# Performance work log

Measured on AMD Instinct MI355X. Metric: run time of the kernel, lower is better.

## Reference

```python
import jax, jax.numpy as jnp
import numpy as np

B, N, K, H = 8, 3072, 20, 64
NT = B * N            # 24576 total nodes
E = NT * 20           # 491520 GAT edges
HEADS = 4
BN_EPS = 1e-5


def setup_inputs() -> dict:
    key = jax.random.key(0)
    ks = jax.random.split(key, 16)
    rn = lambda k, shp, s=0.05: jax.random.normal(k, shp, dtype=jnp.float32) * s
    z = lambda shp: jnp.zeros(shp, dtype=jnp.float32)
    inp = {}
    inp["x"] = jax.random.normal(ks[0], (NT, 8), dtype=jnp.float32)
    inp["batch"] = jnp.repeat(jnp.arange(B, dtype=jnp.int32), N)
    inp["edge_index"] = jax.random.randint(ks[1], (2, E), 0, NT)
    # lc_encode: Linear(8,32) -> ELU -> Linear(32,H) -> ELU
    inp["enc_W1"] = rn(ks[2], (8, 32)); inp["enc_b1"] = z(32)
    inp["enc_W2"] = rn(ks[3], (32, H)); inp["enc_b2"] = z(H)
    # 3 DynamicEdgeConv MLPs: Linear(2H,H) -> ELU -> BatchNorm(eval) -> Dropout(eval=id)
    inp["conv_W"] = rn(ks[4], (3, 2 * H, H)); inp["conv_b"] = z((3, H))
    inp["bn_g"] = jnp.ones((3, H), jnp.float32); inp["bn_b"] = z((3, H))
    inp["bn_m"] = z((3, H)); inp["bn_v"] = jnp.ones((3, H), jnp.float32)
    # 2 GATConv layers: heads=4, concat=False (mean over heads)
    inp["gat_W"] = rn(ks[5], (2, H, HEADS * H))
    inp["gat_asrc"] = rn(ks[6], (2, HEADS, H))
    inp["gat_adst"] = rn(ks[7], (2, HEADS, H))
    inp["gat_bias"] = z((2, H))
    # output MLP: Linear(H,64) ELU Linear(64,32) ELU Linear(32,8)
    inp["out_W1"] = rn(ks[8], (H, 64)); inp["out_b1"] = z(64)
    inp["out_W2"] = rn(ks[9], (64, 32)); inp["out_b2"] = z(32)
    inp["out_W3"] = rn(ks[10], (32, 8)); inp["out_b3"] = z(8)
    return inp


def _knn_idx(x):
    # x: [B,N,H]; k nearest neighbors per graph, excluding self
    sq = jnp.sum(x * x, axis=-1)
    d = sq[:, :, None] + sq[:, None, :] - 2.0 * jnp.einsum('bnh,bmh->bnm', x, x)
    d = d + jnp.eye(N, dtype=x.dtype)[None] * 1e9
    _, idx = jax.lax.top_k(-d, K)
    return idx  # [B,N,K]


def _dyn_edge_conv(x, W, b, g, be, m, v):
    # x: [B,N,H]; EdgeConv message nn([x_i, x_j - x_i]), max-aggr over k neighbors
    idx = _knn_idx(x)
    xj = jax.vmap(lambda xb, ib: xb[ib])(x, idx)          # [B,N,K,H]
    xi = x[:, :, None, :]
    e = jnp.concatenate([jnp.broadcast_to(xi, xj.shape), xj - xi], axis=-1)  # [B,N,K,2H]
    h = jax.nn.elu(jnp.einsum('bnkf,fh->bnkh', e, W) + b)
    h = g * (h - m) * jax.lax.rsqrt(v + BN_EPS) + be      # BatchNorm1d (eval)
    return jnp.max(h, axis=2)                             # [B,N,H]


def _gat(x, ei, W, asrc, adst, bias):
    # x: [NT,H]; PyG GATConv, heads=4, concat=False, with self-loops
    xh = (x @ W).reshape(NT, HEADS, H)
    loops = jnp.arange(NT)
    src = jnp.concatenate([ei[0], loops])
    dst = jnp.concatenate([ei[1], loops])
    al_s = jnp.einsum('nhc,hc->nh', xh, asrc)
    al_d = jnp.einsum('nhc,hc->nh', xh, adst)
    alpha = jax.nn.leaky_relu(al_s[src] + al_d[dst], 0.2)  # [E+NT, HEADS]
    mx = jax.ops.segment_max(alpha, dst, num_segments=NT)
    ea = jnp.exp(alpha - mx[dst])
    den = jax.ops.segment_sum(ea, dst, num_segments=NT)
    a = ea / (den[dst] + 1e-16)
    out = jax.ops.segment_sum(xh[src] * a[:, :, None], dst, num_segments=NT)
    return out.mean(axis=1) + bias                        # concat=False -> head mean


def reference(x, batch, edge_index, enc_W1, enc_b1, enc_W2, enc_b2,
              conv_W, conv_b, bn_g, bn_b, bn_m, bn_v,
              gat_W, gat_asrc, gat_adst, gat_bias,
              out_W1, out_b1, out_W2, out_b2, out_W3, out_b3):
    # lc_encode (dropout layers are identity in eval mode)
    h = jax.nn.elu(jax.nn.elu(x @ enc_W1 + enc_b1) @ enc_W2 + enc_b2)
    hb = h.reshape(B, N, H)  # regular batch: node i belongs to graph i // N
    for i in range(3):
        hb = _dyn_edge_conv(hb, conv_W[i], conv_b[i], bn_g[i], bn_b[i], bn_m[i], bn_v[i]) + hb
    feats = hb.reshape(NT, H)
    x1 = _gat(feats, edge_index, gat_W[0], gat_asrc[0], gat_adst[0], gat_bias[0]) + feats
    x2 = _gat(x1, edge_index, gat_W[1], gat_asrc[1], gat_adst[1], gat_bias[1]) + x1
    o = jax.nn.elu(x2 @ out_W1 + out_b1)
    o = jax.nn.elu(o @ out_W2 + out_b2)
    return o @ out_W3 + out_b3  # [NT, contrastive_dim]
```

## Files before the change

### kernel.cpp

```cpp
#include <hip/hip_runtime.h>
#include <math.h>

#define NTOT  24576
#define NB    8
#define NPB   3072
#define HD    64
#define KNN   20
#define NTILE 24

__device__ __forceinline__ float elu_f(float x){ return x > 0.f ? x : expm1f(x); }

__global__ __launch_bounds__(256) void enc_kernel(const float* __restrict__ x,
    const float* __restrict__ W1, const float* __restrict__ b1,
    const float* __restrict__ W2, const float* __restrict__ b2,
    float* __restrict__ out, float* __restrict__ sqo){
  __shared__ float sW1[256], sb1[32], sW2[2048], sb2[64];
  int t = threadIdx.x;
  if (t < 256) sW1[t] = W1[t];
  for (int i = t; i < 2048; i += 256) sW2[i] = W2[i];
  if (t < 32) sb1[t] = b1[t];
  if (t < 64) sb2[t] = b2[t];
  __syncthreads();
  int n = blockIdx.x*256 + t;
  const float4* xp = (const float4*)(x + (size_t)n*8);
  float4 x0 = xp[0], x1 = xp[1];
  float xi[8] = {x0.x,x0.y,x0.z,x0.w,x1.x,x1.y,x1.z,x1.w};
  float h1[32];
  #pragma unroll
  for (int j = 0; j < 32; j++){
    float a = sb1[j];
    #pragma unroll
    for (int d = 0; d < 8; d++) a = fmaf(xi[d], sW1[d*32+j], a);
    h1[j] = elu_f(a);
  }
  float4* op = (float4*)(out + (size_t)n*64);
  float ssum = 0.f;
  #pragma unroll
  for (int c4 = 0; c4 < 16; c4++){
    float a0 = sb2[c4*4+0], a1 = sb2[c4*4+1], a2 = sb2[c4*4+2], a3 = sb2[c4*4+3];
    #pragma unroll
    for (int d = 0; d < 32; d++){
      float hd = h1[d];
      float4 wv = *(const float4*)&sW2[d*64 + c4*4];
      a0 = fmaf(hd, wv.x, a0); a1 = fmaf(hd, wv.y, a1);
      a2 = fmaf(hd, wv.z, a2); a3 = fmaf(hd, wv.w, a3);
    }
    float4 o; o.x=elu_f(a0); o.y=elu_f(a1); o.z=elu_f(a2); o.w=elu_f(a3);
    ssum = fmaf(o.x,o.x,ssum); ssum = fmaf(o.y,o.y,ssum);
    ssum = fmaf(o.z,o.z,ssum); ssum = fmaf(o.w,o.w,ssum);
    op[c4] = o;
  }
  sqo[n] = ssum;
}

#define CE(va,ia,vb,ib) { bool sw_ = (vb) < (va); float t1_ = sw_?(vb):(va); float t2_ = sw_?(va):(vb); int t3_ = sw_?(ib):(ia); int t4_ = sw_?(ia):(ib); (va)=t1_; (vb)=t2_; (ia)=t3_; (ib)=t4_; }

__global__ __launch_bounds__(256) void disttop_kernel(const float* __restrict__ feat,
    const float* __restrict__ sqn, float* __restrict__ topv, unsigned int* __restrict__ topi){
  __shared__ float As[16][128];
  __shared__ float Bs[16][128];
  int b  = blockIdx.z;
  int m0 = blockIdx.x * 128;
  int q0 = blockIdx.y * 128;
  const float* fb = feat + (size_t)b*NPB*HD;
  int t = threadIdx.x;
  int tx = t & 15, ty = t >> 4;
  float acc[8][8];
  #pragma unroll
  for (int i = 0; i < 8; i++)
    #pragma unroll
    for (int j = 0; j < 8; j++) acc[i][j] = 0.f;
  #pragma unroll 1
  for (int stage = 0; stage < 4; stage++){
    if (stage) __syncthreads();
    {
      int r = t >> 1, dc = (t & 1) * 8;
      const float4* pa = (const float4*)(fb + (size_t)(q0 + r)*HD + stage*16 + dc);
      const float4* pb = (const float4*)(fb + (size_t)(m0 + r)*HD + stage*16 + dc);
      #pragma unroll
      for (int i = 0; i < 2; i++){
        float4 va = pa[i], vb = pb[i];
        int d = dc + i*4;
        As[d][r]=va.x; As[d+1][r]=va.y; As[d+2][r]=va.z; As[d+3][r]=va.w;
        Bs[d][r]=vb.x; Bs[d+1][r]=vb.y; Bs[d+2][r]=vb.z; Bs[d+3][r]=vb.w;
      }
    }
    __syncthreads();
    #pragma unroll 2
    for (int d = 0; d < 16; d++){
      float af[8], bf[8];
      *(float4*)&af[0] = *(const float4*)&As[d][ty*8];
      *(float4*)&af[4] = *(const float4*)&As[d][ty*8+4];
      *(float4*)&bf[0] = *(const float4*)&Bs[d][tx*8];
      *(float4*)&bf[4] = *(const float4*)&Bs[d][tx*8+4];
      #pragma unroll
      for (int i = 0; i < 8; i++)
        #pragma unroll
        for (int j = 0; j < 8; j++)
          acc[i][j] = fmaf(af[i], bf[j], acc[i][j]);
    }
  }
  float sqv[8];
  {
    const float4* sp = (const float4*)(sqn + (size_t)b*NPB + m0 + tx*8);
    float4 sq0 = sp[0], sq1 = sp[1];
    sqv[0]=sq0.x; sqv[1]=sq0.y; sqv[2]=sq0.z; sqv[3]=sq0.w;
    sqv[4]=sq1.x; sqv[5]=sq1.y; sqv[6]=sq1.z; sqv[7]=sq1.w;
  }
  const float INF = 3.4e38f;
  #pragma unroll
  for (int i = 0; i < 8; i++){
    int qg = q0 + ty*8 + i;
    int cex = qg - m0;
    float s0=INF, s1=INF, s2=INF;
    int i0=0, i1=0, i2=0;
    #pragma unroll
    for (int j = 0; j < 8; j++){
      int c = tx*8 + j;
      float v = fmaf(-2.f, acc[i][j], sqv[j]);
      if (c == cex) v = INF;
      bool l2 = v < s2, l1 = v < s1, l0 = v < s0;
      s2 = l1 ? s1 : (l2 ? v : s2);  i2 = l1 ? i1 : (l2 ? c : i2);
      s1 = l0 ? s0 : (l1 ? v : s1);  i1 = l0 ? i0 : (l1 ? c : i1);
      s0 = l0 ? v : s0;              i0 = l0 ? c : i0;
    }
    #pragma unroll
    for (int off = 1; off < 4; off <<= 1){
      float b0 = __shfl_xor(s0,off,64), b1 = __shfl_xor(s1,off,64), b2 = __shfl_xor(s2,off,64);
      int  bj0 = __shfl_xor(i0,off,64), bj1 = __shfl_xor(i1,off,64), bj2 = __shfl_xor(i2,off,64);
      bool c0 = s0 <= b2; float w0 = c0 ? s0 : b2; int x0 = c0 ? i0 : bj2;
      bool c1 = s1 <= b1; float w1 = c1 ? s1 : b1; int x1 = c1 ? i1 : bj1;
      bool c2 = s2 <= b0; float w2 = c2 ? s2 : b0; int x2 = c2 ? i2 : bj0;
      CE(w0,x0,w1,x1); CE(w0,x0,w2,x2); CE(w1,x1,w2,x2);
      s0=w0; s1=w1; s2=w2; i0=x0; i1=x1; i2=x2;
    }
    if ((tx & 3) == 0){
      size_t rb = ((size_t)(b*NTILE + blockIdx.x)*NPB + qg);
      float* vq = topv + rb*12 + (tx >> 2)*3;
      vq[0] = s0; vq[1] = s1; vq[2] = s2;
      topi[rb*4 + (tx >> 2)] = (unsigned)i0 | ((unsigned)i1 << 8);
    }
  }
}

__global__ __launch_bounds__(256) void ksel_kernel(const float* __restrict__ topv,
    const unsigned int* __restrict__ topi, const float* __restrict__ feat,
    const float* __restrict__ sqn, int* __restrict__ idxout){
  __shared__ float cvs[4][72];
  __shared__ int   cxs[4][72];
  int wid = threadIdx.x >> 6, lane = threadIdx.x & 63;
  int g = blockIdx.x*4 + wid;
  int b = g / NPB;
  int ql = g - b*NPB;
  const float INF = 3.4e38f;
  float ma, sa, ta; int ja, ka;
  {
    size_t rb = ((size_t)(b*NTILE + (lane >> 2))*NPB + ql);
    const float* va = topv + rb*12 + (lane & 3)*3;
    ma = va[0]; sa = va[1]; ta = va[2];
    unsigned pk = topi[rb*4 + (lane & 3)];
    ja = (int)(pk & 255u); ka = (int)((pk >> 8) & 255u);
  }
  float mb = INF, sb = INF, tb = INF;
  int jb = 0, kb = 0;
  if (lane < 32){
    int gg = 64 + lane;
    size_t rb = ((size_t)(b*NTILE + (gg >> 2))*NPB + ql);
    const float* vb_ = topv + rb*12 + (gg & 3)*3;
    mb = vb_[0]; sb = vb_[1]; tb = vb_[2];
    unsigned pk = topi[rb*4 + (gg & 3)];
    jb = (int)(pk & 255u); kb = (int)((pk >> 8) & 255u);
  }
  float T;
  {
    float v = fminf(ma, mb);
    #pragma unroll
    for (int k = 2; k <= 64; k <<= 1){
      #pragma unroll
      for (int j = k >> 1; j > 0; j >>= 1){
        float o = __shfl_xor(v, j, 64);
        bool up    = ((lane & k) == 0);
        bool lower = ((lane & j) == 0);
        float mn = fminf(v, o), mx = fmaxf(v, o);
        v = (lower == up) ? mn : mx;
      }
    }
    T = __shfl(v, 19, 64);
  }
  bool cleanA = (ta > T);
  bool cleanB = (tb > T);
  float* cv = cvs[wid]; int* cx = cxs[wid];
  int base = 0;
  {
    bool f = cleanA && (ma <= T);
    unsigned long long mk = __ballot(f);
    int pos = (int)__popcll(mk & ((1ull<<lane)-1ull));
    if (f && pos < 64){ cv[pos] = ma; cx[pos] = (lane>>2)*128 + ja; }
    base = (int)__popcll(mk);
    f = cleanA && (sa <= T);
    mk = __ballot(f);
    pos = base + (int)__popcll(mk & ((1ull<<lane)-1ull));
    if (f && pos < 64){ cv[pos] = sa; cx[pos] = (lane>>2)*128 + ka; }
    base += (int)__popcll(mk);
    f = (lane < 32) && cleanB && (mb <= T);
    mk = __ballot(f);
    pos = base + (int)__popcll(mk & ((1ull<<lane)-1ull));
    if (f && pos < 64){ cv[pos] = mb; cx[pos] = ((64+lane)>>2)*128 + jb; }
    base += (int)__popcll(mk);
    f = (lane < 32) && cleanB && (sb <= T);
    mk = __ballot(f);
    pos = base + (int)__popcll(mk & ((1ull<<lane)-1ull));
    if (f && pos < 64){ cv[pos] = sb; cx[pos] = ((64+lane)>>2)*128 + kb; }
    base += (int)__popcll(mk);
  }
  unsigned long long fa = __ballot(!cleanA);
  unsigned long long fbm = __ballot((lane < 32) && !cleanB);
  const float* fqp = feat + (size_t)g*HD;
  #pragma unroll 1
  for (int w = 0; w < 2; w++){
    unsigned long long fm = (w==0) ? fa : fbm;
    int gofs = (w==0) ? 0 : 64;
    while (fm){
      int p = __ffsll((unsigned long long)fm) - 1; fm &= fm - 1;
      int gg = gofs + p;
      int mbase = (gg >> 2)*128 + (gg & 3)*32;
      bool fire = false; float s = 0.f;
      if (lane < 32){
        int m = mbase + lane;
        const float* fmp = feat + (size_t)(b*NPB + m)*HD;
        float acc = 0.f;
        #pragma unroll
        for (int d4 = 0; d4 < 16; d4++){
          float4 fq4 = *(const float4*)(fqp + d4*4);
          float4 fm4 = *(const float4*)(fmp + d4*4);
          acc = fmaf(fq4.x, fm4.x, acc);
          acc = fmaf(fq4.y, fm4.y, acc);
          acc = fmaf(fq4.z, fm4.z, acc);
          acc = fmaf(fq4.w, fm4.w, acc);
        }
        s = fmaf(-2.f, acc, sqn[(size_t)b*NPB + m]);
        fire = (m != ql) && (s <= T);
      }
      unsigned long long mk2 = __ballot(fire);
      int p2 = base + (int)__popcll(mk2 & ((1ull<<lane)-1ull));
      if (fire && p2 < 64){ cv[p2] = s; cx[p2] = mbase + lane; }
      base += (int)__popcll(mk2);
    }
  }
  if (base <= 64){
    unsigned long long key;
    if (lane < base){
      unsigned int ku = __float_as_uint(cv[lane]);
      ku ^= (unsigned)(((int)ku) >> 31) | 0x80000000u;
      key = ((unsigned long long)ku << 32) | (unsigned int)cx[lane];
    } else key = ~0ull;
    #pragma unroll
    for (int k = 2; k <= 64; k <<= 1){
      #pragma unroll
      for (int j = k >> 1; j > 0; j >>= 1){
        unsigned long long o = __shfl_xor(key, j, 64);
        bool up    = ((lane & k) == 0);
        bool lower = ((lane & j) == 0);
        unsigned long long mn = key < o ? key : o;
        unsigned long long mx = key < o ? o : key;
        key = (lower == up) ? mn : mx;
      }
    }
    if (lane < KNN)
      idxout[(size_t)g*KNN + lane] = b*NPB + (int)(unsigned int)(key & 0xffffffffu);
  } else {
    float dl[KNN]; int il[KNN];
    #pragma unroll
    for (int k = 0; k < KNN; k++){ dl[k] = INF; il[k] = 0x7fffffff; }
    #pragma unroll 1
    for (int j = 0; j < 48; j++){
      int m = j*64 + lane;
      if (m == ql) continue;
      const float* fmp = feat + (size_t)(b*NPB + m)*HD;
      float acc = 0.f;
      for (int d4 = 0; d4 < 16; d4++){
        float4 fq4 = *(const float4*)(fqp + d4*4);
        float4 fm4 = *(const float4*)(fmp + d4*4);
        acc = fmaf(fq4.x, fm4.x, acc);
        acc = fmaf(fq4.y, fm4.y, acc);
        acc = fmaf(fq4.z, fm4.z, acc);
        acc = fmaf(fq4.w, fm4.w, acc);
      }
      float s = fmaf(-2.f, acc, sqn[(size_t)b*NPB + m]);
      if (s < dl[KNN-1]){
        #pragma unroll
        for (int k = KNN-1; k >= 1; k--){
          bool c1 = s < dl[k-1];
          bool c0 = s < dl[k];
          dl[k] = c1 ? dl[k-1] : (c0 ? s : dl[k]);
          il[k] = c1 ? il[k-1] : (c0 ? m : il[k]);
        }
        if (s < dl[0]){ dl[0] = s; il[0] = m; }
      }
    }
    int res = 0;
    #pragma unroll 1
    for (int r = 0; r < KNN; r++){
      float d = dl[0]; int i = il[0];
      #pragma unroll
      for (int off = 1; off < 64; off <<= 1){
        float od = __shfl_xor(d, off, 64);
        int   oi = __shfl_xor(i, off, 64);
        if (od < d || (od == d && oi < i)){ d = od; i = oi; }
      }
      if (lane == r) res = i;
      if (il[0] == i){
        #pragma unroll
        for (int k = 0; k < KNN-1; k++){ dl[k] = dl[k+1]; il[k] = il[k+1]; }
        dl[KNN-1] = INF; il[KNN-1] = 0x7fffffff;
      }
    }
    if (lane < KNN) idxout[(size_t)g*KNN + lane] = b*NPB + res;
  }
}

__global__ __launch_bounds__(256) void uv_kernel(const float* __restrict__ feat,
    const float* __restrict__ W, const float* __restrict__ cb,
    float* __restrict__ u, float* __restrict__ v){
  __shared__ float sW[128*64];
  int t = threadIdx.x;
  for (int i = t; i < 8192; i += 256) sW[i] = W[i];
  __syncthreads();
  int n = blockIdx.x*256 + t;
  float4 fv[16];
  const float4* fp = (const float4*)(feat + (size_t)n*64);
  #pragma unroll
  for (int i = 0; i < 16; i++) fv[i] = fp[i];
  float4* up = (float4*)(u + (size_t)n*64);
  float4* vp = (float4*)(v + (size_t)n*64);
  #pragma unroll 1
  for (int c4 = 0; c4 < 16; c4++){
    float ua0=0,ua1=0,ua2=0,ua3=0, vb0=0,vb1=0,vb2=0,vb3=0;
    #pragma unroll
    for (int d4 = 0; d4 < 16; d4++){
      float4 fq = fv[d4];
      #pragma unroll
      for (int dd = 0; dd < 4; dd++){
        int d = d4*4 + dd;
        float fd = dd==0?fq.x : dd==1?fq.y : dd==2?fq.z : fq.w;
        float4 wt = *(const float4*)&sW[d*64 + c4*4];
        float4 wb = *(const float4*)&sW[(64+d)*64 + c4*4];
        ua0=fmaf(fd,wt.x,ua0); ua1=fmaf(fd,wt.y,ua1); ua2=fmaf(fd,wt.z,ua2); ua3=fmaf(fd,wt.w,ua3);
        vb0=fmaf(fd,wb.x,vb0); vb1=fmaf(fd,wb.y,vb1); vb2=fmaf(fd,wb.z,vb2); vb3=fmaf(fd,wb.w,vb3);
      }
    }
    float4 cbv = *(const float4*)&cb[c4*4];
    float4 uo, vo;
    uo.x = cbv.x + ua0 - vb0; uo.y = cbv.y + ua1 - vb1;
    uo.z = cbv.z + ua2 - vb2; uo.w = cbv.w + ua3 - vb3;
    vo.x = vb0; vo.y = vb1; vo.z = vb2; vo.w = vb3;
    up[c4] = uo; vp[c4] = vo;
  }
}

__global__ __launch_bounds__(256) void pool_kernel(const float* __restrict__ u, const float* __restrict__ v,
    const int* __restrict__ idx, const float* __restrict__ resid,
    const float* __restrict__ bg, const float* __restrict__ bb,
    const float* __restrict__ bm, const float* __restrict__ bv,
    float* __restrict__ out, float* __restrict__ sqo){
  int gid = blockIdx.x*256 + threadIdx.x;
  int n = gid >> 6, lane = gid & 63;
  float uc = u[(size_t)n*64 + lane];
  float scale = bg[lane] / sqrtf(bv[lane] + 1e-5f);
  float bias  = bb[lane] - bm[lane]*scale;
  const int* ip = idx + (size_t)n*KNN;
  float acc = -3.4e38f;
  #pragma unroll 4
  for (int k = 0; k < KNN; k++){
    int j = ip[k];
    float s = uc + v[(size_t)j*64 + lane];
    acc = fmaxf(acc, fmaf(elu_f(s), scale, bias));
  }
  float val = acc + resid[(size_t)n*64 + lane];
  out[(size_t)n*64 + lane] = val;
  float ss = val*val;
  #pragma unroll
  for (int off = 1; off < 64; off <<= 1) ss += __shfl_xor(ss, off, 64);
  if (lane == 0) sqo[n] = ss;
}

__global__ void deg_init(int* deg){ int i = blockIdx.x*256 + threadIdx.x; if (i < NTOT) deg[i] = 1; }
__global__ void deg_hist(const int* __restrict__ ei, int E, int* deg){
  int i = blockIdx.x*256 + threadIdx.x; if (i < E) atomicAdd(&deg[ei[E + i]], 1);
}
__global__ void scan_kernel(const int* __restrict__ deg, int* __restrict__ rowptr, int* __restrict__ cursor){
  __shared__ int part[256];
  int t = threadIdx.x;
  int base = t*96;
  int s = 0;
  for (int i = 0; i < 96; i++) s += deg[base + i];
  part[t] = s;
  __syncthreads();
  for (int off = 1; off < 256; off <<= 1){
    int xv = (t >= off) ? part[t - off] : 0;
    __syncthreads();
    part[t] += xv;
    __syncthreads();
  }
  int run = part[t] - s;
  for (int i = 0; i < 96; i++){
    rowptr[base + i] = run; cursor[base + i] = run; run += deg[base + i];
  }
  if (t == 255) rowptr[NTOT] = run;
}
__global__ void scatter_kernel(const int* __restrict__ ei, int E, int* cursor, int* __restrict__ csr){
  int i = blockIdx.x*256 + threadIdx.x;
  if (i >= E + NTOT) return;
  int s, d;
  if (i < E){ s = ei[i]; d = ei[E + i]; } else { s = i - E; d = s; }
  int pos = atomicAdd(&cursor[d], 1);
  csr[pos] = s;
}

__global__ __launch_bounds__(256) void xh_kernel(const float* __restrict__ feat,
    const float* __restrict__ W, const float* __restrict__ asrc, const float* __restrict__ adst,
    float* __restrict__ xh, float* __restrict__ al){
  __shared__ float sW[64*128];
  __shared__ float sas[256], sad[256];
  int t = threadIdx.x;
  if (t < 256){ sas[t] = asrc[t]; sad[t] = adst[t]; }
  int n = blockIdx.x*256 + t;
  float4 fv[16];
  const float4* fp = (const float4*)(feat + (size_t)n*64);
  #pragma unroll
  for (int i = 0; i < 16; i++) fv[i] = fp[i];
  float4* xp = (float4*)(xh + (size_t)n*256);
  float* ap = al + (size_t)n*8;
  #pragma unroll 1
  for (int half = 0; half < 2; half++){
    __syncthreads();
    for (int i = t; i < 8192; i += 256){
      int d = i >> 7, c = i & 127;
      sW[i] = W[d*256 + half*128 + c];
    }
    __syncthreads();
    #pragma unroll 1
    for (int hh = 0; hh < 2; hh++){
      int h = half*2 + hh;
      float as_ = 0.f, ad_ = 0.f;
      #pragma unroll 1
      for (int cc = 0; cc < 64; cc += 4){
        int c  = h*64 + cc;
        int cl = hh*64 + cc;
        float a0=0,a1=0,a2=0,a3=0;
        #pragma unroll
        for (int d4 = 0; d4 < 16; d4++){
          float4 fq = fv[d4];
          #pragma unroll
          for (int dd = 0; dd < 4; dd++){
            int d = d4*4 + dd;
            float fd = dd==0?fq.x : dd==1?fq.y : dd==2?fq.z : fq.w;
            float4 wv = *(const float4*)&sW[d*128 + cl];
            a0=fmaf(fd,wv.x,a0); a1=fmaf(fd,wv.y,a1); a2=fmaf(fd,wv.z,a2); a3=fmaf(fd,wv.w,a3);
          }
        }
        float4 o; o.x=a0; o.y=a1; o.z=a2; o.w=a3;
        xp[c >> 2] = o;
        as_ = fmaf(a0, sas[c], fmaf(a1, sas[c+1], fmaf(a2, sas[c+2], fmaf(a3, sas[c+3], as_))));
        ad_ = fmaf(a0, sad[c], fmaf(a1, sad[c+1], fmaf(a2, sad[c+2], fmaf(a3, sad[c+3], ad_))));
      }
      ap[h] = as_; ap[4 + h] = ad_;
    }
  }
}

__global__ __launch_bounds__(256) void agg_kernel(const float* __restrict__ xh, const float* __restrict__ al,
    const int* __restrict__ rowptr, const int* __restrict__ csr,
    const float* __restrict__ resid, const float* __restrict__ bias,
    float* __restrict__ out){
  int gid = blockIdx.x*256 + threadIdx.x;
  int n = gid >> 6, lane = gid & 63;
  int rs = rowptr[n], re = rowptr[n+1];
  int h = lane >> 4, coff = (lane & 15)*4;
  float ald_h = al[(size_t)n*8 + 4 + h];
  float mx = -3.4e38f, den = 0.f;
  float ax=0.f, ay=0.f, az=0.f, aw=0.f;
  #pragma unroll 2
  for (int e = rs; e < re; e++){
    int s = csr[e];
    float a = al[(size_t)s*8 + h] + ald_h;
    a = a > 0.f ? a : 0.2f*a;
    float nm = fmaxf(mx, a);
    float corr = __expf(mx - nm);
    float ea   = __expf(a - nm);
    mx = nm;
    float4 xv = *(const float4*)(xh + (size_t)s*256 + h*64 + coff);
    den = fmaf(den, corr, ea);
    ax = fmaf(ax, corr, ea*xv.x); ay = fmaf(ay, corr, ea*xv.y);
    az = fmaf(az, corr, ea*xv.z); aw = fmaf(aw, corr, ea*xv.w);
  }
  float rinv = 1.f / (den + 1e-16f);
  float r0 = ax*rinv, r1 = ay*rinv, r2 = az*rinv, r3 = aw*rinv;
  r0 += __shfl_xor(r0, 16, 64); r1 += __shfl_xor(r1, 16, 64);
  r2 += __shfl_xor(r2, 16, 64); r3 += __shfl_xor(r3, 16, 64);
  r0 += __shfl_xor(r0, 32, 64); r1 += __shfl_xor(r1, 32, 64);
  r2 += __shfl_xor(r2, 32, 64); r3 += __shfl_xor(r3, 32, 64);
  if (lane < 16){
    float4 bs = *(const float4*)(bias + coff);
    float4 rv = *(const float4*)(resid + (size_t)n*64 + coff);
    float4 o;
    o.x = r0*0.25f + bs.x + rv.x; o.y = r1*0.25f + bs.y + rv.y;
    o.z = r2*0.25f + bs.z + rv.z; o.w = r3*0.25f + bs.w + rv.w;
    *(float4*)(out + (size_t)n*64 + coff) = o;
  }
}

__global__ __launch_bounds__(256) void mlp_kernel(const float* __restrict__ feat,
    const float* __restrict__ W1, const float* __restrict__ b1,
    const float* __restrict__ W2, const float* __restrict__ b2,
    const float* __restrict__ W3, const float* __restrict__ b3,
    float* __restrict__ out){
  __shared__ float s1[4096], s2[2048], s3[256], t1[64], t2[32], t3[8];
  int t = threadIdx.x;
  for (int i = t; i < 4096; i += 256) s1[i] = W1[i];
  for (int i = t; i < 2048; i += 256) s2[i] = W2[i];
  if (t < 256) s3[t] = W3[t];
  if (t < 64) t1[t] = b1[t];
  if (t < 32) t2[t] = b2[t];
  if (t < 8)  t3[t] = b3[t];
  __syncthreads();
  int n = blockIdx.x*256 + t;
  float4 fv[16];
  const float4* fp = (const float4*)(feat + (size_t)n*64);
  #pragma unroll
  for (int i = 0; i < 16; i++) fv[i] = fp[i];
  float o1[64];
  #pragma unroll 1
  for (int c4 = 0; c4 < 16; c4++){
    float a0=t1[c4*4+0], a1=t1[c4*4+1], a2=t1[c4*4+2], a3=t1[c4*4+3];
    #pragma unroll
    for (int d4 = 0; d4 < 16; d4++){
      float4 fq = fv[d4];
      #pragma unroll
      for (int dd = 0; dd < 4; dd++){
        int d = d4*4 + dd;
        float fd = dd==0?fq.x : dd==1?fq.y : dd==2?fq.z : fq.w;
        float4 wv = *(const float4*)&s1[d*64 + c4*4];
        a0=fmaf(fd,wv.x,a0); a1=fmaf(fd,wv.y,a1); a2=fmaf(fd,wv.z,a2); a3=fmaf(fd,wv.w,a3);
      }
    }
    o1[c4*4+0]=elu_f(a0); o1[c4*4+1]=elu_f(a1); o1[c4*4+2]=elu_f(a2); o1[c4*4+3]=elu_f(a3);
  }
  float o2[32];
  #pragma unroll 1
  for (int c4 = 0; c4 < 8; c4++){
    float a0=t2[c4*4+0], a1=t2[c4*4+1], a2=t2[c4*4+2], a3=t2[c4*4+3];
    #pragma unroll
    for (int d = 0; d < 64; d++){
      float fd = o1[d];
      float4 wv = *(const float4*)&s2[d*32 + c4*4];
      a0=fmaf(fd,wv.x,a0); a1=fmaf(fd,wv.y,a1); a2=fmaf(fd,wv.z,a2); a3=fmaf(fd,wv.w,a3);
    }
    o2[c4*4+0]=elu_f(a0); o2[c4*4+1]=elu_f(a1); o2[c4*4+2]=elu_f(a2); o2[c4*4+3]=elu_f(a3);
  }
  float4* op = (float4*)(out + (size_t)n*8);
  #pragma unroll
  for (int c4 = 0; c4 < 2; c4++){
    float a0=t3[c4*4+0], a1=t3[c4*4+1], a2=t3[c4*4+2], a3=t3[c4*4+3];
    #pragma unroll
    for (int d = 0; d < 32; d++){
      float fd = o2[d];
      float4 wv = *(const float4*)&s3[d*8 + c4*4];
      a0=fmaf(fd,wv.x,a0); a1=fmaf(fd,wv.y,a1); a2=fmaf(fd,wv.z,a2); a3=fmaf(fd,wv.w,a3);
    }
    float4 o; o.x=a0; o.y=a1; o.z=a2; o.w=a3;
    op[c4] = o;
  }
}

extern "C" void kernel_launch(void* const* d_in, const int* in_sizes, int n_in,
                              void* d_out, int out_size, void* d_ws, size_t ws_size,
                              hipStream_t stream){
  (void)n_in; (void)out_size; (void)ws_size;
  const float* x     = (const float*)d_in[0];
  const int*   ei    = (const int*)d_in[2];
  const int    E     = in_sizes[2] / 2;
  const float* encW1 = (const float*)d_in[3];
  const float* encb1 = (const float*)d_in[4];
  const float* encW2 = (const float*)d_in[5];
  const float* encb2 = (const float*)d_in[6];
  const float* convW = (const float*)d_in[7];
  const float* convb = (const float*)d_in[8];
  const float* bng   = (const float*)d_in[9];
  const float* bnb   = (const float*)d_in[10];
  const float* bnm   = (const float*)d_in[11];
  const float* bnv   = (const float*)d_in[12];
  const float* gatW  = (const float*)d_in[13];
  const float* gatas = (const float*)d_in[14];
  const float* gatad = (const float*)d_in[15];
  const float* gatb  = (const float*)d_in[16];
  const float* oW1   = (const float*)d_in[17];
  const float* ob1   = (const float*)d_in[18];
  const float* oW2   = (const float*)d_in[19];
  const float* ob2   = (const float*)d_in[20];
  const float* oW3   = (const float*)d_in[21];
  const float* ob3   = (const float*)d_in[22];

  char* wp = (char*)d_ws;
  auto alloc = [&](size_t bytes)->void*{
    void* p = (void*)wp; wp += (bytes + 255) & ~((size_t)255); return p;
  };
  float* fA     = (float*)alloc((size_t)NTOT*64*4);
  float* fB     = (float*)alloc((size_t)NTOT*64*4);
  float* ubuf   = (float*)alloc((size_t)NTOT*64*4);
  float* vbuf   = (float*)alloc((size_t)NTOT*64*4);
  float* sqb    = (float*)alloc((size_t)NTOT*4);
  int*   idxb   = (int*)  alloc((size_t)NTOT*KNN*4);
  float* xhb    = (float*)alloc((size_t)NTOT*256*4);
  float* alb    = (float*)alloc((size_t)NTOT*8*4);
  int*   degb   = (int*)  alloc((size_t)NTOT*4);
  int*   rowptr = (int*)  alloc((size_t)(NTOT+1)*4);
  int*   cursor = (int*)  alloc((size_t)NTOT*4);
  int*   csr    = (int*)  alloc((size_t)(E+NTOT)*4);
  float* topv   = (float*)alloc((size_t)NTOT*288*4);
  unsigned int* topi = (unsigned int*)alloc((size_t)NTOT*96*4);

  enc_kernel<<<96,256,0,stream>>>(x, encW1, encb1, encW2, encb2, fA, sqb);
  float* cur = fA; float* nxt = fB;
  for (int l = 0; l < 3; l++){
    disttop_kernel<<<dim3(NTILE,NTILE,NB),256,0,stream>>>(cur, sqb, topv, topi);
    ksel_kernel   <<<NTOT/4,              256,0,stream>>>(topv, topi, cur, sqb, idxb);
    uv_kernel  <<<96,  256,0,stream>>>(cur, convW + (size_t)l*8192, convb + l*64, ubuf, vbuf);
    pool_kernel<<<6144,256,0,stream>>>(ubuf, vbuf, idxb, cur,
                                       bng + l*64, bnb + l*64, bnm + l*64, bnv + l*64, nxt, sqb);
    float* tmp = cur; cur = nxt; nxt = tmp;
  }
  deg_init   <<<96,            256,0,stream>>>(degb);
  deg_hist   <<<(E+255)/256,   256,0,stream>>>(ei, E, degb);
  scan_kernel<<<1,             256,0,stream>>>(degb, rowptr, cursor);
  scatter_kernel<<<(E+NTOT+255)/256,256,0,stream>>>(ei, E, cursor, csr);
  for (int l = 0; l < 2; l++){
    xh_kernel <<<96,  256,0,stream>>>(cur, gatW + (size_t)l*16384, gatas + l*256, gatad + l*256, xhb, alb);
    agg_kernel<<<6144,256,0,stream>>>(xhb, alb, rowptr, csr, cur, gatb + l*64, nxt);
    float* tmp = cur; cur = nxt; nxt = tmp;
  }
  mlp_kernel<<<96,256,0,stream>>>(cur, oW1, ob1, oW2, ob2, oW3, ob3, (float*)d_out);
}
```

Measured before the change: 1.126 ms.

## Exploit distance-matrix symmetry by computing only upper-triangular tile pairs in kNN

The kNN distance/top-k kernel now launches one block per upper-triangular (query tile, candidate tile) pair, 300 instead of 576 per graph. Each off-diagonal block reuses its dot-product accumulator transposed to also produce top-3 candidates for the mirrored tile pair. This is meant to roughly halve the GEMM work and feature loads. In exchange there is a serial loop to decode the tile pair, extra column-wise selection and shuffles, and less even work across blocks.

```diff
diff --git a/kernel.cpp b/kernel.cpp
--- a/kernel.cpp
+++ b/kernel.cpp
@@ -7,6 +7,7 @@
 #define HD    64
 #define KNN   20
 #define NTILE 24
+#define TPAIRS 300
 
 __device__ __forceinline__ float elu_f(float x){ return x > 0.f ? x : expm1f(x); }
 
@@ -59,9 +60,11 @@
     const float* __restrict__ sqn, float* __restrict__ topv, unsigned int* __restrict__ topi){
   __shared__ float As[16][128];
   __shared__ float Bs[16][128];
-  int b  = blockIdx.z;
-  int m0 = blockIdx.x * 128;
-  int q0 = blockIdx.y * 128;
+  int b = blockIdx.z;
+  int L = blockIdx.x, tq = 0;
+  while (L >= NTILE - tq){ L -= NTILE - tq; tq++; }
+  int tm = tq + L;
+  int q0 = tq*128, m0 = tm*128;
   const float* fb = feat + (size_t)b*NPB*HD;
   int t = threadIdx.x;
   int tx = t & 15, ty = t >> 4;
@@ -107,6 +110,13 @@
     sqv[0]=sq0.x; sqv[1]=sq0.y; sqv[2]=sq0.z; sqv[3]=sq0.w;
     sqv[4]=sq1.x; sqv[5]=sq1.y; sqv[6]=sq1.z; sqv[7]=sq1.w;
   }
+  float sqQ[8];
+  {
+    const float4* sp = (const float4*)(sqn + (size_t)b*NPB + q0 + ty*8);
+    float4 sq0 = sp[0], sq1 = sp[1];
+    sqQ[0]=sq0.x; sqQ[1]=sq0.y; sqQ[2]=sq0.z; sqQ[3]=sq0.w;
+    sqQ[4]=sq1.x; sqQ[5]=sq1.y; sqQ[6]=sq1.z; sqQ[7]=sq1.w;
+  }
   const float INF = 3.4e38f;
   #pragma unroll
   for (int i = 0; i < 8; i++){
@@ -135,10 +145,43 @@
       s0=w0; s1=w1; s2=w2; i0=x0; i1=x1; i2=x2;
     }
     if ((tx & 3) == 0){
-      size_t rb = ((size_t)(b*NTILE + blockIdx.x)*NPB + qg);
+      size_t rb = ((size_t)(b*NTILE + tm)*NPB + qg);
       float* vq = topv + rb*12 + (tx >> 2)*3;
       vq[0] = s0; vq[1] = s1; vq[2] = s2;
       topi[rb*4 + (tx >> 2)] = (unsigned)i0 | ((unsigned)i1 << 8);
+    }
+  }
+  if (tm != tq){
+    #pragma unroll
+    for (int j = 0; j < 8; j++){
+      int qc = m0 + tx*8 + j;
+      float s0=INF, s1=INF, s2=INF;
+      int i0=0, i1=0, i2=0;
+      #pragma unroll
+      for (int i = 0; i < 8; i++){
+        int c = ty*8 + i;
+        float v = fmaf(-2.f, acc[i][j], sqQ[i]);
+        bool l2 = v < s2, l1 = v < s1, l0 = v < s0;
+        s2 = l1 ? s1 : (l2 ? v : s2);  i2 = l1 ? i1 : (l2 ? c : i2);
+        s1 = l0 ? s0 : (l1 ? v : s1);  i1 = l0 ? i0 : (l1 ? c : i1);
+        s0 = l0 ? v : s0;              i0 = l0 ? c : i0;
+      }
+      #pragma unroll
+      for (int off = 16; off < 64; off <<= 1){
+        float b0 = __shfl_xor(s0,off,64), b1 = __shfl_xor(s1,off,64), b2 = __shfl_xor(s2,off,64);
+        int  bj0 = __shfl_xor(i0,off,64), bj1 = __shfl_xor(i1,off,64), bj2 = __shfl_xor(i2,off,64);
+        bool c0 = s0 <= b2; float w0 = c0 ? s0 : b2; int x0 = c0 ? i0 : bj2;
+        bool c1 = s1 <= b1; float w1 = c1 ? s1 : b1; int x1 = c1 ? i1 : bj1;
+        bool c2 = s2 <= b0; float w2 = c2 ? s2 : b0; int x2 = c2 ? i2 : bj0;
+        CE(w0,x0,w1,x1); CE(w0,x0,w2,x2); CE(w1,x1,w2,x2);
+        s0=w0; s1=w1; s2=w2; i0=x0; i1=x1; i2=x2;
+      }
+      if ((ty & 3) == 0){
+        size_t rb = ((size_t)(b*NTILE + tq)*NPB + qc);
+        float* vq = topv + rb*12 + (ty >> 2)*3;
+        vq[0] = s0; vq[1] = s1; vq[2] = s2;
+        topi[rb*4 + (ty >> 2)] = (unsigned)i0 | ((unsigned)i1 << 8);
+      }
     }
   }
 }
@@ -623,7 +666,7 @@
   enc_kernel<<<96,256,0,stream>>>(x, encW1, encb1, encW2, encb2, fA, sqb);
   float* cur = fA; float* nxt = fB;
   for (int l = 0; l < 3; l++){
-    disttop_kernel<<<dim3(NTILE,NTILE,NB),256,0,stream>>>(cur, sqb, topv, topi);
+    disttop_kernel<<<dim3(TPAIRS,1,NB),256,0,stream>>>(cur, sqb, topv, topi);
     ksel_kernel   <<<NTOT/4,              256,0,stream>>>(topv, topi, cur, sqb, idxb);
     uv_kernel  <<<96,  256,0,stream>>>(cur, convW + (size_t)l*8192, convb + l*64, ubuf, vbuf);
     pool_kernel<<<6144,256,0,stream>>>(ubuf, vbuf, idxb, cur,
```

Measured after the change: 1.008 ms, median of 2. 10.5% less time.
